# Kernel tuning notes

Measured on AMD Instinct MI355X. Metric: run time of the kernel, lower is better.

Reference implementation:

```python
import jax, jax.numpy as jnp
import numpy as np

EMBED = 1024
HEADS = 16


def setup_inputs() -> dict:
    key = jax.random.key(0)
    ks = jax.random.split(key, 12)
    N, S, E = 8, 1024, EMBED
    s = 1.0 / np.sqrt(E)
    inp = {
        'queries': jax.random.normal(ks[0], (N, S, E), jnp.float32),
        'keys': jax.random.normal(ks[1], (N, S, E), jnp.float32),
        'values': jax.random.normal(ks[2], (N, S, E), jnp.float32),
        'Wq': jax.random.normal(ks[3], (E, E), jnp.float32) * s,
        'bq': jax.random.normal(ks[4], (E,), jnp.float32) * s,
        'Wk': jax.random.normal(ks[5], (E, E), jnp.float32) * s,
        'bk': jax.random.normal(ks[6], (E,), jnp.float32) * s,
        'Wv': jax.random.normal(ks[7], (E, E), jnp.float32) * s,
        'bv': jax.random.normal(ks[8], (E,), jnp.float32) * s,
        'Wo': jax.random.normal(ks[9], (E, E), jnp.float32) * s,
        'bo': jax.random.normal(ks[10], (E,), jnp.float32) * s,
    }
    return inp


def reference(queries, keys, values, Wq, bq, Wk, bk, Wv, bv, Wo, bo):
    N, S, E = queries.shape
    H = HEADS
    D = E // H
    # linear projections (torch Linear: x @ W.T + b)
    q = queries @ Wq.T + bq
    k = keys @ Wk.T + bk
    v = values @ Wv.T + bv
    q = q.reshape(N, S, H, D)
    k = k.reshape(N, S, H, D)
    v = v.reshape(N, S, H, D)
    # NOTE: original scales by sqrt(embed_size), not sqrt(head_dim)
    scores = jnp.einsum('nqhd,nkhd->nhqk', q, k) / jnp.sqrt(jnp.float32(E))
    attn = jax.nn.softmax(scores, axis=3)
    out = jnp.einsum('nhqk,nkhd->nqhd', attn, v).reshape(N, S, E)
    return out @ Wo.T + bo
```

## Files before the change

### kernel.cpp

```cpp
#include <hip/hip_runtime.h>


typedef unsigned short ushort_t;
typedef __bf16 bf16_8 __attribute__((ext_vector_type(8)));
typedef float f32x4 __attribute__((ext_vector_type(4)));
typedef unsigned short ushort8 __attribute__((ext_vector_type(8)));
typedef short short8v __attribute__((ext_vector_type(8)));

#define SEQ  1024
#define EMB  1024
#define NBAT 8
#define NH   16
#define HD   64
#define MROW (NBAT * SEQ)

__device__ __forceinline__ ushort_t cvt_bf16(float x) {
  unsigned u = __float_as_uint(x);
  u += 0x7FFFu + ((u >> 16) & 1u);
  return (ushort_t)(u >> 16);
}
__device__ __forceinline__ float bf2f(ushort_t u) {
  return __uint_as_float(((unsigned)u) << 16);
}
__device__ __forceinline__ short f2bs(float x) {
  return __builtin_bit_cast(short, (__bf16)x);
}

__device__ __forceinline__ void async_copy16(const ushort_t* g, ushort_t* l) {
  __builtin_amdgcn_global_load_lds(
      (const __attribute__((address_space(1))) void*)g,
      (__attribute__((address_space(3))) void*)l, 16, 0, 0);
}

__global__ void dtype_probe(const ushort_t* __restrict__ w, int* __restrict__ flag) {
  __shared__ int cnt;
  if (threadIdx.x == 0) cnt = 0;
  __syncthreads();
  int c = 0;
  for (int i = threadIdx.x; i < 4096; i += 256) {
    const int e = (w[i] >> 7) & 0xFF;
    if (e >= 129) ++c;
  }
  atomicAdd(&cnt, c);
  __syncthreads();
  if (threadIdx.x == 0) *flag = (cnt > 256) ? 1 : 0;
}

__device__ __forceinline__ ushort8 load8(const void* base, size_t off, bool f32) {
  if (f32) {
    const float* p = (const float*)base + off;
    const f32x4 a = *(const f32x4*)p;
    const f32x4 b = *(const f32x4*)(p + 4);
    ushort8 r;
    r[0] = cvt_bf16(a[0]); r[1] = cvt_bf16(a[1]);
    r[2] = cvt_bf16(a[2]); r[3] = cvt_bf16(a[3]);
    r[4] = cvt_bf16(b[0]); r[5] = cvt_bf16(b[1]);
    r[6] = cvt_bf16(b[2]); r[7] = cvt_bf16(b[3]);
    return r;
  }
  return *(const ushort8*)((const ushort_t*)base + off);
}

__global__ __launch_bounds__(256)
void convert_all(const void* __restrict__ q, const void* __restrict__ k,
                 const void* __restrict__ v, const void* __restrict__ wq,
                 const void* __restrict__ wk, const void* __restrict__ wv,
                 const void* __restrict__ wo,
                 ushort_t* __restrict__ cq, ushort_t* __restrict__ ck,
                 ushort_t* __restrict__ cv, ushort_t* __restrict__ cwq,
                 ushort_t* __restrict__ cwk, ushort_t* __restrict__ cwv,
                 ushort_t* __restrict__ cwo, const int* __restrict__ flag) {
  const bool f32 = (*flag != 0);
  const int b = blockIdx.x;
  const void* src;
  ushort_t* dst;
  int boff;
  if (b < 12288) {
    const int t = b >> 12;
    boff = b & 4095;
    src = (t == 0) ? q : (t == 1) ? k : v;
    dst = (t == 0) ? cq : (t == 1) ? ck : cv;
  } else {
    const int t = (b - 12288) >> 9;
    boff = (b - 12288) & 511;
    src = (t == 0) ? wq : (t == 1) ? wk : (t == 2) ? wv : wo;
    dst = (t == 0) ? cwq : (t == 1) ? cwk : (t == 2) ? cwv : cwo;
  }
  const size_t i = (size_t)boff * 256 + threadIdx.x;
  *(ushort8*)(dst + i * 8) = load8(src, i * 8, f32);
}

__device__ __forceinline__ void gemm_body(
    ushort_t* As, ushort_t* Bs,
    const ushort_t* __restrict__ A, const ushort_t* __restrict__ B,
    const void* __restrict__ bias, void* __restrict__ Cout, bool f32,
    int bm, int bn, int mode) {
  const int tid  = threadIdx.x;
  const int lane = tid & 63;
  const int wave = tid >> 6;
  const int wm = wave & 1, wn = wave >> 1;
  const int col  = lane & 15;
  const int quad = lane >> 4;

  const ushort_t* Ab = A + (size_t)bm * EMB;
  const ushort_t* Bb = B + (size_t)bn * EMB;

  float bvv[4];
  if (mode != 1) {
#pragma unroll
    for (int nt = 0; nt < 4; ++nt) {
      const int i = bn + wn * 64 + nt * 16 + col;
      bvv[nt] = f32 ? ((const float*)bias)[i] : bf2f(((const ushort_t*)bias)[i]);
    }
  }

  f32x4 acc[4][4] = {};

  for (int kb = 0; kb < EMB; kb += 64) {
#pragma unroll
    for (int j = 0; j < 4; ++j) {
      const int s   = j * 256 + tid;
      const int row = s >> 3;
      const int ch  = (s & 7) << 3;
      const int s0  = j * 256 + wave * 64;
      async_copy16(Ab + (size_t)row * EMB + kb + ch, &As[s0 * 8]);
      async_copy16(Bb + (size_t)row * EMB + kb + ch, &Bs[s0 * 8]);
    }
    __syncthreads();

#pragma unroll
    for (int kk = 0; kk < 2; ++kk) {
      bf16_8 af[4], bfr[4];
#pragma unroll
      for (int mt = 0; mt < 4; ++mt)
        af[mt] = *(const bf16_8*)(As + (wm * 64 + mt * 16 + col) * 64 +
                                  kk * 32 + quad * 8);
#pragma unroll
      for (int nt = 0; nt < 4; ++nt)
        bfr[nt] = *(const bf16_8*)(Bs + (wn * 64 + nt * 16 + col) * 64 +
                                   kk * 32 + quad * 8);
#pragma unroll
      for (int mt = 0; mt < 4; ++mt)
#pragma unroll
        for (int nt = 0; nt < 4; ++nt)
          acc[mt][nt] = __builtin_amdgcn_mfma_f32_16x16x32_bf16(af[mt], bfr[nt],
                                                                acc[mt][nt], 0, 0, 0);
    }
    __syncthreads();
  }

#pragma unroll
  for (int mt = 0; mt < 4; ++mt)
#pragma unroll
    for (int nt = 0; nt < 4; ++nt) {
      const int gcol = bn + wn * 64 + nt * 16 + col;
#pragma unroll
      for (int r = 0; r < 4; ++r) {
        const int grow = bm + wm * 64 + mt * 16 + quad * 4 + r;
        if (mode == 1) {
          const float bb =
              f32 ? ((const float*)bias)[grow] : bf2f(((const ushort_t*)bias)[grow]);
          const float vv = acc[mt][nt][r] + bb;
          const int nn = gcol >> 10, ss = gcol & 1023;
          const int hh = grow >> 6,  dd = grow & 63;
          ((ushort_t*)Cout)[(size_t)((nn * NH + hh) * HD + dd) * SEQ + ss] =
              cvt_bf16(vv);
        } else {
          const float vv = acc[mt][nt][r] + bvv[nt];
          const size_t idx = (size_t)grow * EMB + gcol;
          if (mode == 2 && f32) ((float*)Cout)[idx] = vv;
          else                  ((ushort_t*)Cout)[idx] = cvt_bf16(vv);
        }
      }
    }
}

__global__ __launch_bounds__(256)
void gemm_qkv(const ushort_t* __restrict__ cq, const ushort_t* __restrict__ ck,
              const ushort_t* __restrict__ cv, const ushort_t* __restrict__ cWq,
              const ushort_t* __restrict__ cWk, const ushort_t* __restrict__ cWv,
              const void* __restrict__ bq, const void* __restrict__ bk,
              const void* __restrict__ bv, void* __restrict__ Qp,
              void* __restrict__ Kp, void* __restrict__ Vt,
              const int* __restrict__ flag) {
  __shared__ __align__(16) ushort_t As[128 * 64];
  __shared__ __align__(16) ushort_t Bs[128 * 64];
  const bool f32 = (*flag != 0);
  const int t = blockIdx.x >> 9;
  const int bid = blockIdx.x & 511;
  if (t == 0)
    gemm_body(As, Bs, cq, cWq, bq, Qp, f32, (bid & 63) << 7, (bid >> 6) << 7, 0);
  else if (t == 1)
    gemm_body(As, Bs, ck, cWk, bk, Kp, f32, (bid & 63) << 7, (bid >> 6) << 7, 0);
  else
    gemm_body(As, Bs, cWv, cv, bv, Vt, f32, (bid & 7) << 7, (bid >> 3) << 7, 1);
}

__global__ __launch_bounds__(256)
void gemm_one(const ushort_t* __restrict__ A, const ushort_t* __restrict__ B,
              const void* __restrict__ bias, void* __restrict__ Cout,
              const int* __restrict__ flag, int mode) {
  __shared__ __align__(16) ushort_t As[128 * 64];
  __shared__ __align__(16) ushort_t Bs[128 * 64];
  gemm_body(As, Bs, A, B, bias, Cout, (*flag != 0),
            (blockIdx.x & 63) << 7, (blockIdx.x >> 6) << 7, mode);
}

template <int MODE>
__global__ __launch_bounds__(256)
void gemm_flex(const void* __restrict__ A, const void* __restrict__ B,
               const void* __restrict__ bias, void* __restrict__ Cout,
               const int* __restrict__ flag, int a_ext, int final_out) {
  __shared__ __align__(16) ushort_t As[128 * 32];
  __shared__ __align__(16) ushort_t Bs[128 * 32];
  const bool f32  = (*flag != 0);
  const bool af32 = f32 && (a_ext != 0);
  const int tid  = threadIdx.x;
  const int lane = tid & 63;
  const int wave = tid >> 6;
  const int wm = wave & 1, wn = wave >> 1;
  const int col  = lane & 15;
  const int quad = lane >> 4;
  const int bm = (blockIdx.x & 63) << 7;
  const int bn = (blockIdx.x >> 6) << 7;

  f32x4 acc[4][4] = {};

  for (int kb = 0; kb < EMB; kb += 32) {
    ushort8 ra[2], rb[2];
#pragma unroll
    for (int j = 0; j < 2; ++j) {
      const int s   = j * 256 + tid;
      const int row = s >> 2;
      const int ch  = (s & 3) << 3;
      ra[j] = load8(A, (size_t)(bm + row) * EMB + kb + ch, af32);
      rb[j] = load8(B, (size_t)(bn + row) * EMB + kb + ch, f32);
    }
#pragma unroll
    for (int j = 0; j < 2; ++j) {
      const int s = j * 256 + tid;
      *(ushort8*)(As + s * 8) = ra[j];
      *(ushort8*)(Bs + s * 8) = rb[j];
    }
    __syncthreads();

    bf16_8 af[4], bfr[4];
#pragma unroll
    for (int mt = 0; mt < 4; ++mt)
      af[mt] = *(const bf16_8*)(As + (wm * 64 + mt * 16 + col) * 32 + quad * 8);
#pragma unroll
    for (int nt = 0; nt < 4; ++nt)
      bfr[nt] = *(const bf16_8*)(Bs + (wn * 64 + nt * 16 + col) * 32 + quad * 8);
#pragma unroll
    for (int mt = 0; mt < 4; ++mt)
#pragma unroll
      for (int nt = 0; nt < 4; ++nt)
        acc[mt][nt] = __builtin_amdgcn_mfma_f32_16x16x32_bf16(af[mt], bfr[nt],
                                                              acc[mt][nt], 0, 0, 0);
    __syncthreads();
  }

  float bvv[4];
#pragma unroll
  for (int nt = 0; nt < 4; ++nt) {
    const int i = bn + wn * 64 + nt * 16 + col;
    bvv[nt] = f32 ? ((const float*)bias)[i] : bf2f(((const ushort_t*)bias)[i]);
  }
#pragma unroll
  for (int mt = 0; mt < 4; ++mt)
#pragma unroll
    for (int nt = 0; nt < 4; ++nt) {
      const int gcol = bn + wn * 64 + nt * 16 + col;
#pragma unroll
      for (int r = 0; r < 4; ++r) {
        const int grow = bm + wm * 64 + mt * 16 + quad * 4 + r;
        const float vv = acc[mt][nt][r] + bvv[nt];
        if (MODE == 0) {
          const size_t idx = (size_t)grow * EMB + gcol;
          if (final_out && f32) ((float*)Cout)[idx] = vv;
          else                  ((ushort_t*)Cout)[idx] = cvt_bf16(vv);
        } else {
          const int nn = grow >> 10, ss = grow & 1023;
          const int hh = gcol >> 6,  dd = gcol & 63;
          ((ushort_t*)Cout)[(size_t)((nn * NH + hh) * HD + dd) * SEQ + ss] =
              cvt_bf16(vv);
        }
      }
    }
}

__global__ __launch_bounds__(256)
void attn_kernel(const ushort_t* __restrict__ Q, const ushort_t* __restrict__ K,
                 const ushort_t* __restrict__ V, ushort_t* __restrict__ O) {
  const int tid  = threadIdx.x;
  const int lane = tid & 63;
  const int wave = tid >> 6;
  const int col  = lane & 15;
  const int quad = lane >> 4;
  const int gid = blockIdx.x;
  const int nh  = gid & 127;
  const int qb  = gid >> 7;
  const int h  = nh & 15;
  const int n  = nh >> 4;
  const int q0 = qb * 256 + wave * 64;

  bf16_8 aq0[4], aq1[4];
#pragma unroll
  for (int g = 0; g < 4; ++g) {
    const ushort_t* qp =
        Q + (size_t)(n * SEQ + q0 + g * 16 + col) * EMB + h * HD + quad * 8;
    aq0[g] = *(const bf16_8*)qp;
    aq1[g] = *(const bf16_8*)(qp + 32);
  }

  const int sig = ((col >> 2) << 3) | (col & 3);
  const ushort_t* kp = K + (size_t)(n * SEQ + sig) * EMB + h * HD + quad * 8;
  const ushort_t* vp = V + ((size_t)nh * HD + col) * SEQ + quad * 8;

  f32x4 acc[4][4] = {};
  float lsum[4] = {0.f, 0.f, 0.f, 0.f};

  const float SCL = 0.04508422f;
  const float MOF = 16.0f;

#define ATTN_LOAD(KX, VX, KB_)                                               \
  do {                                                                       \
    const ushort_t* kpi = kp + (size_t)(KB_) * EMB;                          \
    KX[0] = *(const bf16_8*)(kpi);                                           \
    KX[1] = *(const bf16_8*)(kpi + 32);                                      \
    KX[2] = *(const bf16_8*)(kpi + 4 * EMB);                                 \
    KX[3] = *(const bf16_8*)(kpi + 4 * EMB + 32);                            \
    _Pragma("unroll")                                                        \
    for (int dt = 0; dt < 4; ++dt)                                           \
      VX[dt] = *(const bf16_8*)(vp + (size_t)dt * 16 * SEQ + (KB_));         \
  } while (0)

#define ATTN_TILE(KX, VX)                                                    \
  do {                                                                       \
    _Pragma("unroll")                                                        \
    for (int g = 0; g < 4; ++g) {                                            \
      const f32x4 z = {};                                                    \
      __builtin_amdgcn_s_setprio(1);                                         \
      f32x4 s0 = __builtin_amdgcn_mfma_f32_16x16x32_bf16(KX[0], aq0[g], z, 0, 0, 0); \
      s0 = __builtin_amdgcn_mfma_f32_16x16x32_bf16(KX[1], aq1[g], s0, 0, 0, 0);      \
      f32x4 s1 = __builtin_amdgcn_mfma_f32_16x16x32_bf16(KX[2], aq0[g], z, 0, 0, 0); \
      s1 = __builtin_amdgcn_mfma_f32_16x16x32_bf16(KX[3], aq1[g], s1, 0, 0, 0);      \
      __builtin_amdgcn_s_setprio(0);                                         \
      short8v pas;                                                           \
      _Pragma("unroll")                                                      \
      for (int r = 0; r < 4; ++r) {                                          \
        const float p0 = __builtin_amdgcn_exp2f(__builtin_fmaf(s0[r], SCL, -MOF)); \
        const float p1 = __builtin_amdgcn_exp2f(__builtin_fmaf(s1[r], SCL, -MOF)); \
        lsum[g] += p0 + p1;                                                  \
        pas[r]     = f2bs(p0);                                               \
        pas[r + 4] = f2bs(p1);                                               \
      }                                                                      \
      const bf16_8 pab = __builtin_bit_cast(bf16_8, pas);                    \
      __builtin_amdgcn_s_setprio(1);                                         \
      _Pragma("unroll")                                                      \
      for (int dt = 0; dt < 4; ++dt)                                         \
        acc[g][dt] = __builtin_amdgcn_mfma_f32_16x16x32_bf16(pab, VX[dt], acc[g][dt], 0, 0, 0); \
      __builtin_amdgcn_s_setprio(0);                                         \
    }                                                                        \
  } while (0)

  bf16_8 K0[4], K1[4], K2[4], V0[4], V1[4], V2[4];

  ATTN_LOAD(K0, V0, 0);
  ATTN_LOAD(K1, V1, 32);
  ATTN_LOAD(K2, V2, 64);
  __builtin_amdgcn_sched_barrier(0);

  for (int t = 0; t < 30; t += 3) {
    ATTN_TILE(K0, V0);
    if (t + 3 < 32) { ATTN_LOAD(K0, V0, (t + 3) * 32); __builtin_amdgcn_sched_barrier(0); }
    ATTN_TILE(K1, V1);
    if (t + 4 < 32) { ATTN_LOAD(K1, V1, (t + 4) * 32); __builtin_amdgcn_sched_barrier(0); }
    ATTN_TILE(K2, V2);
    if (t + 5 < 32) { ATTN_LOAD(K2, V2, (t + 5) * 32); __builtin_amdgcn_sched_barrier(0); }
  }
  ATTN_TILE(K0, V0);
  ATTN_TILE(K1, V1);

#undef ATTN_LOAD
#undef ATTN_TILE

#pragma unroll
  for (int g = 0; g < 4; ++g) {
    float tot = lsum[g];
    tot += __shfl_xor(tot, 16, 64);
    tot += __shfl_xor(tot, 32, 64);
    float rinv[4];
#pragma unroll
    for (int r = 0; r < 4; ++r)
      rinv[r] = 1.0f / __shfl(tot, quad * 4 + r, 16);
#pragma unroll
    for (int dt = 0; dt < 4; ++dt)
#pragma unroll
      for (int r = 0; r < 4; ++r)
        O[(size_t)(n * SEQ + q0 + g * 16 + quad * 4 + r) * EMB + h * HD +
          dt * 16 + col] = cvt_bf16(acc[g][dt][r] * rinv[r]);
  }
}

extern "C" void kernel_launch(void* const* d_in, const int* in_sizes, int n_in,
                              void* d_out, int out_size, void* d_ws, size_t ws_size,
                              hipStream_t stream) {
  const void* q  = d_in[0];
  const void* k  = d_in[1];
  const void* v  = d_in[2];
  const void* Wq = d_in[3];
  const void* bq = d_in[4];
  const void* Wk = d_in[5];
  const void* bk = d_in[6];
  const void* Wv = d_in[7];
  const void* bv = d_in[8];
  const void* Wo = d_in[9];
  const void* bo = d_in[10];

  const size_t TE = (size_t)MROW * EMB;
  const size_t WE = (size_t)EMB * EMB;
  int* flag = (int*)d_ws;
  char* base = (char*)d_ws + 256;
  const size_t NEED = 256 + (4 * TE + 4 * WE) * sizeof(ushort_t);

  const dim3 tB(256);
  dtype_probe<<<dim3(1), tB, 0, stream>>>((const ushort_t*)Wq, flag);

  if (ws_size >= NEED) {
    ushort_t* cq  = (ushort_t*)base;
    ushort_t* ck  = cq + TE;
    ushort_t* cv  = ck + TE;
    ushort_t* Qp  = cv + TE;
    ushort_t* cWq = Qp + TE;
    ushort_t* cWk = cWq + WE;
    ushort_t* cWv = cWk + WE;
    ushort_t* cWo = cWv + WE;
    ushort_t* Kp  = (ushort_t*)d_out;
    ushort_t* Vt  = (ushort_t*)d_out + TE;
    ushort_t* Oa  = Qp;

    convert_all<<<dim3(14336), tB, 0, stream>>>(q, k, v, Wq, Wk, Wv, Wo,
                                                cq, ck, cv, cWq, cWk, cWv, cWo,
                                                flag);
    gemm_qkv<<<dim3(1536), tB, 0, stream>>>(cq, ck, cv, cWq, cWk, cWv,
                                            bq, bk, bv, Qp, Kp, Vt, flag);
    attn_kernel<<<dim3(512), tB, 0, stream>>>(Qp, Kp, Vt, Oa);
    gemm_one<<<dim3(512), tB, 0, stream>>>(Oa, cWo, bo, d_out, flag, 2);
  } else {
    ushort_t* Qp = (ushort_t*)base;
    ushort_t* Vt = Qp + TE;
    ushort_t* Kp = (ushort_t*)d_out;
    ushort_t* Oa = Qp;
    const dim3 gB(512);
    gemm_flex<0><<<gB, tB, 0, stream>>>(q, Wq, bq, Qp, flag, 1, 0);
    gemm_flex<0><<<gB, tB, 0, stream>>>(k, Wk, bk, Kp, flag, 1, 0);
    gemm_flex<1><<<gB, tB, 0, stream>>>(v, Wv, bv, Vt, flag, 1, 0);
    attn_kernel<<<dim3(512), tB, 0, stream>>>(Qp, Kp, Vt, Oa);
    gemm_flex<0><<<gB, tB, 0, stream>>>(Oa, Wo, bo, d_out, flag, 0, 1);
  }
}
```

Baseline: 355.0 us.

## Fuse activation fp32-to-bf16 conversion into QKV GEMM loads, merge dtype probe

Stops converting the q/k/v activations to bf16 in a separate pass. The QKV GEMM now loads fp32 activations through registers, converts them, and writes bf16 into LDS. This removes a full write and re-read of three 8M-element bf16 copies. The dtype probe is folded into the weight-conversion kernel, and the GEMM K-tile shrinks from 64 to 32 to fit the register-staged path. The cost is synchronous register-staged loads on the activation side and twice as many K iterations and barriers.

```diff
diff --git a/kernel.cpp b/kernel.cpp
--- a/kernel.cpp
+++ b/kernel.cpp
@@ -62,39 +62,38 @@
 }
 
 __global__ __launch_bounds__(256)
-void convert_all(const void* __restrict__ q, const void* __restrict__ k,
-                 const void* __restrict__ v, const void* __restrict__ wq,
-                 const void* __restrict__ wk, const void* __restrict__ wv,
-                 const void* __restrict__ wo,
-                 ushort_t* __restrict__ cq, ushort_t* __restrict__ ck,
-                 ushort_t* __restrict__ cv, ushort_t* __restrict__ cwq,
-                 ushort_t* __restrict__ cwk, ushort_t* __restrict__ cwv,
-                 ushort_t* __restrict__ cwo, const int* __restrict__ flag) {
-  const bool f32 = (*flag != 0);
-  const int b = blockIdx.x;
-  const void* src;
-  ushort_t* dst;
-  int boff;
-  if (b < 12288) {
-    const int t = b >> 12;
-    boff = b & 4095;
-    src = (t == 0) ? q : (t == 1) ? k : v;
-    dst = (t == 0) ? cq : (t == 1) ? ck : cv;
-  } else {
-    const int t = (b - 12288) >> 9;
-    boff = (b - 12288) & 511;
-    src = (t == 0) ? wq : (t == 1) ? wk : (t == 2) ? wv : wo;
-    dst = (t == 0) ? cwq : (t == 1) ? cwk : (t == 2) ? cwv : cwo;
-  }
+void convert_w(const ushort_t* __restrict__ wprobe,
+               const void* __restrict__ wq, const void* __restrict__ wk,
+               const void* __restrict__ wv, const void* __restrict__ wo,
+               ushort_t* __restrict__ cwq, ushort_t* __restrict__ cwk,
+               ushort_t* __restrict__ cwv, ushort_t* __restrict__ cwo,
+               int* __restrict__ flag) {
+  __shared__ int cnt;
+  if (threadIdx.x == 0) cnt = 0;
+  __syncthreads();
+  int c = 0;
+  for (int i = threadIdx.x; i < 4096; i += 256) {
+    const int e = (wprobe[i] >> 7) & 0xFF;
+    if (e >= 129) ++c;
+  }
+  atomicAdd(&cnt, c);
+  __syncthreads();
+  const bool f32 = (cnt > 256);
+  if (blockIdx.x == 0 && threadIdx.x == 0) *flag = f32 ? 1 : 0;
+
+  const int t = blockIdx.x >> 9;
+  const int boff = blockIdx.x & 511;
+  const void* src = (t == 0) ? wq : (t == 1) ? wk : (t == 2) ? wv : wo;
+  ushort_t* dst   = (t == 0) ? cwq : (t == 1) ? cwk : (t == 2) ? cwv : cwo;
   const size_t i = (size_t)boff * 256 + threadIdx.x;
   *(ushort8*)(dst + i * 8) = load8(src, i * 8, f32);
 }
 
 __device__ __forceinline__ void gemm_body(
     ushort_t* As, ushort_t* Bs,
-    const ushort_t* __restrict__ A, const ushort_t* __restrict__ B,
+    const void* __restrict__ A, const void* __restrict__ B,
     const void* __restrict__ bias, void* __restrict__ Cout, bool f32,
-    int bm, int bn, int mode) {
+    int bm, int bn, int mode, int a_ext, int b_ext) {
   const int tid  = threadIdx.x;
   const int lane = tid & 63;
   const int wave = tid >> 6;
@@ -102,9 +101,6 @@
   const int col  = lane & 15;
   const int quad = lane >> 4;
 
-  const ushort_t* Ab = A + (size_t)bm * EMB;
-  const ushort_t* Bb = B + (size_t)bn * EMB;
-
   float bvv[4];
   if (mode != 1) {
 #pragma unroll
@@ -116,36 +112,69 @@
 
   f32x4 acc[4][4] = {};
 
-  for (int kb = 0; kb < EMB; kb += 64) {
-#pragma unroll
-    for (int j = 0; j < 4; ++j) {
-      const int s   = j * 256 + tid;
-      const int row = s >> 3;
-      const int ch  = (s & 7) << 3;
-      const int s0  = j * 256 + wave * 64;
-      async_copy16(Ab + (size_t)row * EMB + kb + ch, &As[s0 * 8]);
-      async_copy16(Bb + (size_t)row * EMB + kb + ch, &Bs[s0 * 8]);
+  for (int kb = 0; kb < EMB; kb += 32) {
+    ushort8 ra[2], rb[2];
+    if (a_ext) {
+#pragma unroll
+      for (int j = 0; j < 2; ++j) {
+        const int s = j * 256 + tid, row = s >> 2, ch = (s & 3) << 3;
+        ra[j] = load8(A, (size_t)(bm + row) * EMB + kb + ch, f32);
+      }
+    }
+    if (b_ext) {
+#pragma unroll
+      for (int j = 0; j < 2; ++j) {
+        const int s = j * 256 + tid, row = s >> 2, ch = (s & 3) << 3;
+        rb[j] = load8(B, (size_t)(bn + row) * EMB + kb + ch, f32);
+      }
+    }
+    if (!a_ext) {
+#pragma unroll
+      for (int j = 0; j < 2; ++j) {
+        const int s = j * 256 + tid, row = s >> 2, ch = (s & 3) << 3;
+        const int s0 = j * 256 + wave * 64;
+        async_copy16((const ushort_t*)A + (size_t)(bm + row) * EMB + kb + ch,
+                     &As[s0 * 8]);
+      }
+    }
+    if (!b_ext) {
+#pragma unroll
+      for (int j = 0; j < 2; ++j) {
+        const int s = j * 256 + tid, row = s >> 2, ch = (s & 3) << 3;
+        const int s0 = j * 256 + wave * 64;
+        async_copy16((const ushort_t*)B + (size_t)(bn + row) * EMB + kb + ch,
+                     &Bs[s0 * 8]);
+      }
+    }
+    if (a_ext) {
+#pragma unroll
+      for (int j = 0; j < 2; ++j) {
+        const int s = j * 256 + tid;
+        *(ushort8*)(As + s * 8) = ra[j];
+      }
+    }
+    if (b_ext) {
+#pragma unroll
+      for (int j = 0; j < 2; ++j) {
+        const int s = j * 256 + tid;
+        *(ushort8*)(Bs + s * 8) = rb[j];
+      }
     }
     __syncthreads();
 
-#pragma unroll
-    for (int kk = 0; kk < 2; ++kk) {
-      bf16_8 af[4], bfr[4];
-#pragma unroll
-      for (int mt = 0; mt < 4; ++mt)
-        af[mt] = *(const bf16_8*)(As + (wm * 64 + mt * 16 + col) * 64 +
-                                  kk * 32 + quad * 8);
+    bf16_8 af[4], bfr[4];
+#pragma unroll
+    for (int mt = 0; mt < 4; ++mt)
+      af[mt] = *(const bf16_8*)(As + (wm * 64 + mt * 16 + col) * 32 + quad * 8);
+#pragma unroll
+    for (int nt = 0; nt < 4; ++nt)
+      bfr[nt] = *(const bf16_8*)(Bs + (wn * 64 + nt * 16 + col) * 32 + quad * 8);
+#pragma unroll
+    for (int mt = 0; mt < 4; ++mt)
 #pragma unroll
       for (int nt = 0; nt < 4; ++nt)
-        bfr[nt] = *(const bf16_8*)(Bs + (wn * 64 + nt * 16 + col) * 64 +
-                                   kk * 32 + quad * 8);
-#pragma unroll
-      for (int mt = 0; mt < 4; ++mt)
-#pragma unroll
-        for (int nt = 0; nt < 4; ++nt)
-          acc[mt][nt] = __builtin_amdgcn_mfma_f32_16x16x32_bf16(af[mt], bfr[nt],
-                                                                acc[mt][nt], 0, 0, 0);
-    }
+        acc[mt][nt] = __builtin_amdgcn_mfma_f32_16x16x32_bf16(af[mt], bfr[nt],
+                                                              acc[mt][nt], 0, 0, 0);
     __syncthreads();
   }
 
@@ -176,34 +205,37 @@
 }
 
 __global__ __launch_bounds__(256)
-void gemm_qkv(const ushort_t* __restrict__ cq, const ushort_t* __restrict__ ck,
-              const ushort_t* __restrict__ cv, const ushort_t* __restrict__ cWq,
+void gemm_qkv(const void* __restrict__ q, const void* __restrict__ k,
+              const void* __restrict__ v, const ushort_t* __restrict__ cWq,
               const ushort_t* __restrict__ cWk, const ushort_t* __restrict__ cWv,
               const void* __restrict__ bq, const void* __restrict__ bk,
               const void* __restrict__ bv, void* __restrict__ Qp,
               void* __restrict__ Kp, void* __restrict__ Vt,
               const int* __restrict__ flag) {
-  __shared__ __align__(16) ushort_t As[128 * 64];
-  __shared__ __align__(16) ushort_t Bs[128 * 64];
+  __shared__ __align__(16) ushort_t As[128 * 32];
+  __shared__ __align__(16) ushort_t Bs[128 * 32];
   const bool f32 = (*flag != 0);
   const int t = blockIdx.x >> 9;
   const int bid = blockIdx.x & 511;
   if (t == 0)
-    gemm_body(As, Bs, cq, cWq, bq, Qp, f32, (bid & 63) << 7, (bid >> 6) << 7, 0);
+    gemm_body(As, Bs, q, cWq, bq, Qp, f32, (bid & 63) << 7, (bid >> 6) << 7,
+              0, 1, 0);
   else if (t == 1)
-    gemm_body(As, Bs, ck, cWk, bk, Kp, f32, (bid & 63) << 7, (bid >> 6) << 7, 0);
+    gemm_body(As, Bs, k, cWk, bk, Kp, f32, (bid & 63) << 7, (bid >> 6) << 7,
+              0, 1, 0);
   else
-    gemm_body(As, Bs, cWv, cv, bv, Vt, f32, (bid & 7) << 7, (bid >> 3) << 7, 1);
+    gemm_body(As, Bs, cWv, v, bv, Vt, f32, (bid & 7) << 7, (bid >> 3) << 7,
+              1, 0, 1);
 }
 
 __global__ __launch_bounds__(256)
 void gemm_one(const ushort_t* __restrict__ A, const ushort_t* __restrict__ B,
               const void* __restrict__ bias, void* __restrict__ Cout,
               const int* __restrict__ flag, int mode) {
-  __shared__ __align__(16) ushort_t As[128 * 64];
-  __shared__ __align__(16) ushort_t Bs[128 * 64];
+  __shared__ __align__(16) ushort_t As[128 * 32];
+  __shared__ __align__(16) ushort_t Bs[128 * 32];
   gemm_body(As, Bs, A, B, bias, Cout, (*flag != 0),
-            (blockIdx.x & 63) << 7, (blockIdx.x >> 6) << 7, mode);
+            (blockIdx.x & 63) << 7, (blockIdx.x >> 6) << 7, mode, 0, 0);
 }
 
 template <int MODE>
@@ -422,16 +454,12 @@
   const size_t WE = (size_t)EMB * EMB;
   int* flag = (int*)d_ws;
   char* base = (char*)d_ws + 256;
-  const size_t NEED = 256 + (4 * TE + 4 * WE) * sizeof(ushort_t);
+  const size_t NEED = 256 + (TE + 4 * WE) * sizeof(ushort_t);
 
   const dim3 tB(256);
-  dtype_probe<<<dim3(1), tB, 0, stream>>>((const ushort_t*)Wq, flag);
 
   if (ws_size >= NEED) {
-    ushort_t* cq  = (ushort_t*)base;
-    ushort_t* ck  = cq + TE;
-    ushort_t* cv  = ck + TE;
-    ushort_t* Qp  = cv + TE;
+    ushort_t* Qp  = (ushort_t*)base;
     ushort_t* cWq = Qp + TE;
     ushort_t* cWk = cWq + WE;
     ushort_t* cWv = cWk + WE;
@@ -440,10 +468,9 @@
     ushort_t* Vt  = (ushort_t*)d_out + TE;
     ushort_t* Oa  = Qp;
 
-    convert_all<<<dim3(14336), tB, 0, stream>>>(q, k, v, Wq, Wk, Wv, Wo,
-                                                cq, ck, cv, cWq, cWk, cWv, cWo,
-                                                flag);
-    gemm_qkv<<<dim3(1536), tB, 0, stream>>>(cq, ck, cv, cWq, cWk, cWv,
+    convert_w<<<dim3(2048), tB, 0, stream>>>((const ushort_t*)Wq, Wq, Wk, Wv, Wo,
+                                             cWq, cWk, cWv, cWo, flag);
+    gemm_qkv<<<dim3(1536), tB, 0, stream>>>(q, k, v, cWq, cWk, cWv,
                                             bq, bk, bv, Qp, Kp, Vt, flag);
     attn_kernel<<<dim3(512), tB, 0, stream>>>(Qp, Kp, Vt, Oa);
     gemm_one<<<dim3(512), tB, 0, stream>>>(Oa, cWo, bo, d_out, flag, 2);
@@ -453,6 +480,7 @@
     ushort_t* Kp = (ushort_t*)d_out;
     ushort_t* Oa = Qp;
     const dim3 gB(512);
+    dtype_probe<<<dim3(1), tB, 0, stream>>>((const ushort_t*)Wq, flag);
     gemm_flex<0><<<gB, tB, 0, stream>>>(q, Wq, bq, Qp, flag, 1, 0);
     gemm_flex<0><<<gB, tB, 0, stream>>>(k, Wk, bk, Kp, flag, 1, 0);
     gemm_flex<1><<<gB, tB, 0, stream>>>(v, Wv, bv, Vt, flag, 1, 0);
```

New measurement: 385.3 us. 1.09x slower.

## Fold dtype probe into convert kernel and shrink GEMM K-tile with XOR swizzle

Applied to the files above, without the earlier changes.

The separate single-block dtype probe launch is removed from the main path. Instead, every block of convert_all redundantly scans part of Wq to decide the input dtype, and block 0 writes the flag for later kernels. The shared GEMM body drops its K tile from 64 to 32 and applies an XOR swizzle to the LDS chunk layout to avoid bank conflicts, halving LDS use per block, which may raise occupancy. The trade-offs are twice as many barriers per K loop and extra redundant global reads of Wq in every conversion block.

```diff
diff --git a/kernel.cpp b/kernel.cpp
--- a/kernel.cpp
+++ b/kernel.cpp
@@ -69,8 +69,23 @@
                  ushort_t* __restrict__ cq, ushort_t* __restrict__ ck,
                  ushort_t* __restrict__ cv, ushort_t* __restrict__ cwq,
                  ushort_t* __restrict__ cwk, ushort_t* __restrict__ cwv,
-                 ushort_t* __restrict__ cwo, const int* __restrict__ flag) {
-  const bool f32 = (*flag != 0);
+                 ushort_t* __restrict__ cwo, int* __restrict__ flag) {
+  __shared__ int cnt;
+  if (threadIdx.x == 0) cnt = 0;
+  __syncthreads();
+  {
+    const ushort_t* wp = (const ushort_t*)wq;
+    int c = 0;
+    for (int i = threadIdx.x; i < 4096; i += 256) {
+      const int e = (wp[i] >> 7) & 0xFF;
+      if (e >= 129) ++c;
+    }
+    atomicAdd(&cnt, c);
+  }
+  __syncthreads();
+  const bool f32 = (cnt > 256);
+  if (blockIdx.x == 0 && threadIdx.x == 0) *flag = f32 ? 1 : 0;
+
   const int b = blockIdx.x;
   const void* src;
   ushort_t* dst;
@@ -101,6 +116,7 @@
   const int wm = wave & 1, wn = wave >> 1;
   const int col  = lane & 15;
   const int quad = lane >> 4;
+  const int px   = quad ^ (col & 3);
 
   const ushort_t* Ab = A + (size_t)bm * EMB;
   const ushort_t* Bb = B + (size_t)bn * EMB;
@@ -116,36 +132,31 @@
 
   f32x4 acc[4][4] = {};
 
-  for (int kb = 0; kb < EMB; kb += 64) {
-#pragma unroll
-    for (int j = 0; j < 4; ++j) {
+  for (int kb = 0; kb < EMB; kb += 32) {
+#pragma unroll
+    for (int j = 0; j < 2; ++j) {
       const int s   = j * 256 + tid;
-      const int row = s >> 3;
-      const int ch  = (s & 7) << 3;
+      const int row = s >> 2;
+      const int ch  = (s & 3) ^ (row & 3);
       const int s0  = j * 256 + wave * 64;
-      async_copy16(Ab + (size_t)row * EMB + kb + ch, &As[s0 * 8]);
-      async_copy16(Bb + (size_t)row * EMB + kb + ch, &Bs[s0 * 8]);
+      async_copy16(Ab + (size_t)row * EMB + kb + ch * 8, &As[s0 * 8]);
+      async_copy16(Bb + (size_t)row * EMB + kb + ch * 8, &Bs[s0 * 8]);
     }
     __syncthreads();
 
-#pragma unroll
-    for (int kk = 0; kk < 2; ++kk) {
-      bf16_8 af[4], bfr[4];
-#pragma unroll
-      for (int mt = 0; mt < 4; ++mt)
-        af[mt] = *(const bf16_8*)(As + (wm * 64 + mt * 16 + col) * 64 +
-                                  kk * 32 + quad * 8);
+    bf16_8 af[4], bfr[4];
+#pragma unroll
+    for (int mt = 0; mt < 4; ++mt)
+      af[mt] = *(const bf16_8*)(As + (wm * 64 + mt * 16 + col) * 32 + px * 8);
+#pragma unroll
+    for (int nt = 0; nt < 4; ++nt)
+      bfr[nt] = *(const bf16_8*)(Bs + (wn * 64 + nt * 16 + col) * 32 + px * 8);
+#pragma unroll
+    for (int mt = 0; mt < 4; ++mt)
 #pragma unroll
       for (int nt = 0; nt < 4; ++nt)
-        bfr[nt] = *(const bf16_8*)(Bs + (wn * 64 + nt * 16 + col) * 64 +
-                                   kk * 32 + quad * 8);
-#pragma unroll
-      for (int mt = 0; mt < 4; ++mt)
-#pragma unroll
-        for (int nt = 0; nt < 4; ++nt)
-          acc[mt][nt] = __builtin_amdgcn_mfma_f32_16x16x32_bf16(af[mt], bfr[nt],
-                                                                acc[mt][nt], 0, 0, 0);
-    }
+        acc[mt][nt] = __builtin_amdgcn_mfma_f32_16x16x32_bf16(af[mt], bfr[nt],
+                                                              acc[mt][nt], 0, 0, 0);
     __syncthreads();
   }
 
@@ -183,8 +194,8 @@
               const void* __restrict__ bv, void* __restrict__ Qp,
               void* __restrict__ Kp, void* __restrict__ Vt,
               const int* __restrict__ flag) {
-  __shared__ __align__(16) ushort_t As[128 * 64];
-  __shared__ __align__(16) ushort_t Bs[128 * 64];
+  __shared__ __align__(16) ushort_t As[128 * 32];
+  __shared__ __align__(16) ushort_t Bs[128 * 32];
   const bool f32 = (*flag != 0);
   const int t = blockIdx.x >> 9;
   const int bid = blockIdx.x & 511;
@@ -200,8 +211,8 @@
 void gemm_one(const ushort_t* __restrict__ A, const ushort_t* __restrict__ B,
               const void* __restrict__ bias, void* __restrict__ Cout,
               const int* __restrict__ flag, int mode) {
-  __shared__ __align__(16) ushort_t As[128 * 64];
-  __shared__ __align__(16) ushort_t Bs[128 * 64];
+  __shared__ __align__(16) ushort_t As[128 * 32];
+  __shared__ __align__(16) ushort_t Bs[128 * 32];
   gemm_body(As, Bs, A, B, bias, Cout, (*flag != 0),
             (blockIdx.x & 63) << 7, (blockIdx.x >> 6) << 7, mode);
 }
@@ -425,7 +436,6 @@
   const size_t NEED = 256 + (4 * TE + 4 * WE) * sizeof(ushort_t);
 
   const dim3 tB(256);
-  dtype_probe<<<dim3(1), tB, 0, stream>>>((const ushort_t*)Wq, flag);
 
   if (ws_size >= NEED) {
     ushort_t* cq  = (ushort_t*)base;
@@ -453,6 +463,7 @@
     ushort_t* Kp = (ushort_t*)d_out;
     ushort_t* Oa = Qp;
     const dim3 gB(512);
+    dtype_probe<<<dim3(1), tB, 0, stream>>>((const ushort_t*)Wq, flag);
     gemm_flex<0><<<gB, tB, 0, stream>>>(q, Wq, bq, Qp, flag, 1, 0);
     gemm_flex<0><<<gB, tB, 0, stream>>>(k, Wk, bk, Kp, flag, 1, 0);
     gemm_flex<1><<<gB, tB, 0, stream>>>(v, Wv, bv, Vt, flag, 1, 0);
```

After: 349.6 us. Within noise of the previous version (-1.5%).
